# Kernel tuning notes

Measured on AMD Instinct MI355X. Metric: run time of the kernel, lower is better.

Reference implementation:

```python
import jax, jax.numpy as jnp
import numpy as np

DECAY = 0.9
BETA_OBS = 1.0
BETA_STATE = 1.0

N_OBS = 20000
N_STATES = 1024
N_ACTIONS = 64
STATE_DIM = 256
RFD = 2048


def setup_inputs() -> dict:
    key = jax.random.key(0)
    ks = jax.random.split(key, 7)
    Q = jax.random.normal(ks[0], (STATE_DIM, N_STATES), dtype=jnp.float32) / np.sqrt(STATE_DIM).astype(np.float32)
    V = jax.random.normal(ks[1], (STATE_DIM, N_ACTIONS), dtype=jnp.float32) / np.sqrt(STATE_DIM).astype(np.float32)
    W = jax.random.normal(ks[2], (RFD, STATE_DIM), dtype=jnp.float32)
    M_re = jax.random.normal(ks[3], (RFD, N_OBS), dtype=jnp.float32)
    M_im = jax.random.normal(ks[4], (RFD, N_OBS), dtype=jnp.float32)
    obs = jax.random.uniform(ks[5], (N_OBS,), dtype=jnp.float32)
    action = jax.random.uniform(ks[6], (N_ACTIONS,), dtype=jnp.float32)
    return {"Q": Q, "V": V, "W": W, "M_re": M_re, "M_im": M_im, "obs": obs, "action": action}


def reference(Q, V, W, M_re, M_im, obs, action):
    # One fused POCML step: memory write (decayed outer product), state
    # rotation via complex random-feature phase, clean_up (state-kernel
    # softmax retrieval), and obs retrieval from memory.
    D = W.shape[0]  # random_feature_dim
    M = M_re + 1j * M_im                       # [D, n_obs] complex64
    obs_c = obs.astype(jnp.complex64)
    # get_state_from_memory
    state0 = M @ obs_c                         # [D]
    # update_memory: M *= decay; M += outer(state, obs)
    M_new = DECAY * M + jnp.outer(state0, obs_c)
    # update_state: v = V @ action; phi_v = exp(1j * W @ v); state *= phi_v
    v = V @ action                             # [state_dim]
    phi_v = jnp.exp(1j * (W @ v))              # [D] complex64
    state1 = state0 * phi_v
    # clean_up: phi_Q = exp(1j * W @ Q), weights = softmax(beta*sim(phi_Q.T, state))
    phi_Q = jnp.exp(1j * (W @ Q))              # [D, n_states]
    score = BETA_STATE * (phi_Q.T @ jnp.conj(state1)).real / D  # [n_states]
    weights = jax.nn.softmax(score)
    state2 = phi_Q @ weights.astype(jnp.complex64)              # [D]
    # get_obs_from_memory: softmax(beta_obs * sim(M.T, state))
    obs_score = BETA_OBS * (M_new.T @ jnp.conj(state2)).real / D  # [n_obs]
    return jax.nn.softmax(obs_score)
```

## Files before the change

kernel.cpp:

```cpp
#include <hip/hip_runtime.h>
#include <math.h>

#define N_OBS    20000
#define N_OBS8   2500
#define N_STATES 1024
#define N_ACT    64
#define SDIM     256
#define RFD      2048
#define DECAY    0.9f
#define HALF_O8  1250
#define FLTMAX   3.402823466e+38f

typedef float v4f __attribute__((ext_vector_type(4)));
typedef float v2f __attribute__((ext_vector_type(2)));

__device__ __forceinline__ v4f ntload4(const float* p) {
    return __builtin_nontemporal_load((const v4f*)p);
}

__device__ __forceinline__ unsigned pk4_fp8(float a, float b, float c, float d) {
    unsigned w = __builtin_amdgcn_cvt_pk_fp8_f32(a, b, 0u, false);
    w = __builtin_amdgcn_cvt_pk_fp8_f32(c, d, w, true);
    return w;
}

#define OFF_SCORE  0
#define OFF_OBSACC 1024
#define OFF_DOT0   21024
#define ZERO_CNT   21028
#define OFF_P0RE   21028
#define OFF_P0IM   (OFF_P0RE + 2*RFD)
#define OFF_S2RE   (OFF_P0IM + 2*RFD)
#define OFF_S2IM   (OFF_S2RE + RFD)
#define OFF_VWS    (OFF_S2IM + RFD)
#define OFF_COSQ   (OFF_VWS + SDIM)
#define OFF_SINQ   (OFF_COSQ + RFD*N_STATES)
#define OFF_MH8    (OFF_SINQ + RFD*N_STATES)
#define MH8_FLOATS (RFD * N_OBS8 * 4)
#define WS_FLOATS  (OFF_MH8 + MH8_FLOATS)

#define NB_GEMM   512
#define NB_Z      21
#define NB_P1     (RFD * 2)
#define NB_FUSED  (NB_GEMM + 1 + NB_Z + NB_P1)

__global__ __launch_bounds__(256) void k_fused(
    const float* __restrict__ Mre, const float* __restrict__ Mim,
    const float* __restrict__ obs,
    const float* __restrict__ W, const float* __restrict__ Q,
    const float* __restrict__ V, const float* __restrict__ action,
    float* __restrict__ cosQ, float* __restrict__ sinQ,
    float* __restrict__ p0re, float* __restrict__ p0im,
    float* __restrict__ vout, uint4* __restrict__ Mh8,
    float* __restrict__ zbase)
{
    const int b = blockIdx.x;
    const int tid = threadIdx.x;

    if (b < NB_GEMM) {
        __shared__ float As[16][65];
        __shared__ float Bs[16][64];
        const int tx = tid & 15;
        const int ty = tid >> 4;
        const int m0 = (b >> 4) * 64;
        const int n0 = (b & 15) * 64;
        float c[4][4] = {};
        for (int k0 = 0; k0 < SDIM; k0 += 16) {
            {
                int k = tid & 15, mb = tid >> 4;
                #pragma unroll
                for (int j = 0; j < 4; j++)
                    As[k][mb + 16*j] = W[(size_t)(m0 + mb + 16*j) * SDIM + k0 + k];
            }
            {
                int n = tid & 63, kb = tid >> 6;
                #pragma unroll
                for (int j = 0; j < 4; j++)
                    Bs[kb + 4*j][n] = Q[(size_t)(k0 + kb + 4*j) * N_STATES + n0 + n];
            }
            __syncthreads();
            #pragma unroll
            for (int kk = 0; kk < 16; kk++) {
                float a[4], bb[4];
                #pragma unroll
                for (int i = 0; i < 4; i++) a[i] = As[kk][ty*4 + i];
                #pragma unroll
                for (int j = 0; j < 4; j++) bb[j] = Bs[kk][tx*4 + j];
                #pragma unroll
                for (int i = 0; i < 4; i++)
                    #pragma unroll
                    for (int j = 0; j < 4; j++)
                        c[i][j] += a[i] * bb[j];
            }
            __syncthreads();
        }
        #pragma unroll
        for (int i = 0; i < 4; i++) {
            int d = m0 + ty*4 + i;
            #pragma unroll
            for (int j = 0; j < 4; j++) {
                int s = n0 + tx*4 + j;
                float sn, cs;
                sincosf(c[i][j], &sn, &cs);
                cosQ[(size_t)d * N_STATES + s] = cs;
                sinQ[(size_t)d * N_STATES + s] = sn;
            }
        }
    } else if (b == NB_GEMM) {
        float acc = 0.f;
        for (int a = 0; a < N_ACT; a++) acc += V[tid * N_ACT + a] * action[a];
        vout[tid] = acc;
    } else if (b < NB_GEMM + 1 + NB_Z) {
        int idx = (b - (NB_GEMM + 1)) * 256 + tid;
        if (idx < ZERO_CNT / 4)
            ((float4*)zbase)[idx] = make_float4(0.f, 0.f, 0.f, 0.f);
    } else {
        const int p = b - (NB_GEMM + 1 + NB_Z);
        const int d = p >> 1;
        const int h = p & 1;
        const float* mr = Mre + (size_t)d * N_OBS;
        const float* mi = Mim + (size_t)d * N_OBS;
        uint4* mh = Mh8 + (size_t)d * N_OBS8;
        const float4* ob = (const float4*)obs;
        const int base = h * HALF_O8, lim = base + HALF_O8;
        float ar0 = 0.f, ar1 = 0.f, ai0 = 0.f, ai1 = 0.f;
        int i = base + tid;
        #pragma unroll
        for (int it = 0; it < 5; ++it, i += 256) {
            int ic = i < lim ? i : lim - 1;
            float4 oa = ob[2*ic], obv = ob[2*ic + 1];
            v4f ra = ntload4(mr + 8 * (size_t)ic);
            v4f rb = ntload4(mr + 8 * (size_t)ic + 4);
            v4f qa = ntload4(mi + 8 * (size_t)ic);
            v4f qb = ntload4(mi + 8 * (size_t)ic + 4);
            if (i < lim) {
                uint4 u;
                u.x = pk4_fp8(ra.x, qa.x, ra.y, qa.y);
                u.y = pk4_fp8(ra.z, qa.z, ra.w, qa.w);
                u.z = pk4_fp8(rb.x, qb.x, rb.y, qb.y);
                u.w = pk4_fp8(rb.z, qb.z, rb.w, qb.w);
                mh[ic] = u;
                ar0 += ra.x*oa.x + ra.y*oa.y + ra.z*oa.z + ra.w*oa.w;
                ar1 += rb.x*obv.x + rb.y*obv.y + rb.z*obv.z + rb.w*obv.w;
                ai0 += qa.x*oa.x + qa.y*oa.y + qa.z*oa.z + qa.w*oa.w;
                ai1 += qb.x*obv.x + qb.y*obv.y + qb.z*obv.z + qb.w*obv.w;
            }
        }
        float arr = ar0 + ar1;
        float aii = ai0 + ai1;
        #pragma unroll
        for (int off = 32; off > 0; off >>= 1) {
            arr += __shfl_down(arr, off);
            aii += __shfl_down(aii, off);
        }
        __shared__ float pr[4], pi[4];
        const int wave = tid >> 6, lane = tid & 63;
        if (lane == 0) { pr[wave] = arr; pi[wave] = aii; }
        __syncthreads();
        if (tid == 0) {
            p0re[h * RFD + d] = pr[0] + pr[1] + pr[2] + pr[3];
            p0im[h * RFD + d] = pi[0] + pi[1] + pi[2] + pi[3];
        }
    }
}

__global__ __launch_bounds__(256) void k_score(
    const float* __restrict__ cosQ, const float* __restrict__ sinQ,
    const float* __restrict__ W, const float* __restrict__ vws,
    const float* __restrict__ p0re, const float* __restrict__ p0im,
    float* __restrict__ score)
{
    __shared__ float s1r_s[32], s1i_s[32];
    const int tid = threadIdx.x;
    const int d0 = blockIdx.y * 32;
    {
        const int r = tid >> 3, g = tid & 7;
        const float4* wv4 = (const float4*)(W + (size_t)(d0 + r) * SDIM + g * 32);
        const float4* vv4 = (const float4*)(vws + g * 32);
        float th = 0.f;
        #pragma unroll
        for (int j = 0; j < 8; j++) {
            float4 wv = wv4[j], vv = vv4[j];
            th += wv.x*vv.x + wv.y*vv.y + wv.z*vv.z + wv.w*vv.w;
        }
        th += __shfl_xor(th, 4);
        th += __shfl_xor(th, 2);
        th += __shfl_xor(th, 1);
        if (g == 0) {
            const int d = d0 + r;
            float re = p0re[d] + p0re[RFD + d];
            float im = p0im[d] + p0im[RFD + d];
            float sn, cs;
            sincosf(th, &sn, &cs);
            s1r_s[r] = re * cs - im * sn;
            s1i_s[r] = re * sn + im * cs;
        }
    }
    __syncthreads();
    const int s = blockIdx.x * 256 + tid;
    float acc = 0.f;
    #pragma unroll 4
    for (int j = 0; j < 32; j++) {
        int d = d0 + j;
        acc += cosQ[(size_t)d * N_STATES + s] * s1r_s[j]
             + sinQ[(size_t)d * N_STATES + s] * s1i_s[j];
    }
    atomicAdd(&score[s], acc);
}

__global__ __launch_bounds__(256) void k_wst2(
    const float* __restrict__ cosQ, const float* __restrict__ sinQ,
    const float* __restrict__ score,
    const float* __restrict__ p0re, const float* __restrict__ p0im,
    float* __restrict__ s2re, float* __restrict__ s2im,
    float* __restrict__ dot0)
{
    __shared__ float red[256];
    __shared__ float r1[256], r2[256];
    const int b = blockIdx.x;
    const int tid = threadIdx.x;
    const float scale = 1.f / (float)RFD;
    float4 v = ((const float4*)score)[tid];
    v.x *= scale; v.y *= scale; v.z *= scale; v.w *= scale;
    float mx = fmaxf(fmaxf(v.x, v.y), fmaxf(v.z, v.w));
    red[tid] = mx; __syncthreads();
    for (int s = 128; s > 0; s >>= 1) {
        if (tid < s) red[tid] = fmaxf(red[tid], red[tid+s]);
        __syncthreads();
    }
    mx = red[0]; __syncthreads();
    float4 e;
    e.x = expf(v.x - mx); e.y = expf(v.y - mx);
    e.z = expf(v.z - mx); e.w = expf(v.w - mx);
    red[tid] = e.x + e.y + e.z + e.w; __syncthreads();
    for (int s = 128; s > 0; s >>= 1) {
        if (tid < s) red[tid] += red[tid+s];
        __syncthreads();
    }
    const float inv = 1.f / red[0];
    e.x *= inv; e.y *= inv; e.z *= inv; e.w *= inv;
    __syncthreads();
    float blockdot = 0.f;
    #pragma unroll
    for (int r = 0; r < 2; r++) {
        const int d = b * 2 + r;
        float4 a = ((const float4*)(cosQ + (size_t)d * N_STATES))[tid];
        float4 bb = ((const float4*)(sinQ + (size_t)d * N_STATES))[tid];
        r1[tid] = a.x*e.x + a.y*e.y + a.z*e.z + a.w*e.w;
        r2[tid] = bb.x*e.x + bb.y*e.y + bb.z*e.z + bb.w*e.w;
        __syncthreads();
        for (int s = 128; s > 0; s >>= 1) {
            if (tid < s) { r1[tid] += r1[tid+s]; r2[tid] += r2[tid+s]; }
            __syncthreads();
        }
        if (tid == 0) {
            s2re[d] = r1[0]; s2im[d] = r2[0];
            float s0r = p0re[d] + p0re[RFD + d];
            float s0i = p0im[d] + p0im[RFD + d];
            blockdot += s0r * r1[0] + s0i * r2[0];
        }
        __syncthreads();
    }
    if (tid == 0) atomicAdd(dot0, blockdot);
}

__global__ __launch_bounds__(256) void k_obs_acc8(
    const uint4* __restrict__ Mh8,
    const float* __restrict__ s2re, const float* __restrict__ s2im,
    float* __restrict__ obs_acc)
{
    __shared__ float c_s[32], s_s[32];
    const int tid = threadIdx.x;
    const int dbase = blockIdx.y * 32;
    if (tid < 32) { c_s[tid] = s2re[dbase + tid]; s_s[tid] = s2im[dbase + tid]; }
    __syncthreads();
    const int idx = blockIdx.x * 256 + tid;
    if (idx >= N_OBS8) return;
    const uint4* p = Mh8 + (size_t)dbase * N_OBS8 + idx;
    float a0 = 0.f, a1 = 0.f, a2 = 0.f, a3 = 0.f;
    float a4 = 0.f, a5 = 0.f, a6 = 0.f, a7 = 0.f;
    #pragma unroll 4
    for (int j = 0; j < 32; ++j) {
        uint4 u = p[(size_t)j * N_OBS8];
        float cc = c_s[j], ss = s_s[j];
        v2f f0 = __builtin_amdgcn_cvt_pk_f32_fp8(u.x, false);
        v2f f1 = __builtin_amdgcn_cvt_pk_f32_fp8(u.x, true);
        v2f f2 = __builtin_amdgcn_cvt_pk_f32_fp8(u.y, false);
        v2f f3 = __builtin_amdgcn_cvt_pk_f32_fp8(u.y, true);
        v2f f4 = __builtin_amdgcn_cvt_pk_f32_fp8(u.z, false);
        v2f f5 = __builtin_amdgcn_cvt_pk_f32_fp8(u.z, true);
        v2f f6 = __builtin_amdgcn_cvt_pk_f32_fp8(u.w, false);
        v2f f7 = __builtin_amdgcn_cvt_pk_f32_fp8(u.w, true);
        a0 += f0.x*cc + f0.y*ss;
        a1 += f1.x*cc + f1.y*ss;
        a2 += f2.x*cc + f2.y*ss;
        a3 += f3.x*cc + f3.y*ss;
        a4 += f4.x*cc + f4.y*ss;
        a5 += f5.x*cc + f5.y*ss;
        a6 += f6.x*cc + f6.y*ss;
        a7 += f7.x*cc + f7.y*ss;
    }
    float* dst = obs_acc + idx * 8;
    atomicAdd(dst + 0, a0);
    atomicAdd(dst + 1, a1);
    atomicAdd(dst + 2, a2);
    atomicAdd(dst + 3, a3);
    atomicAdd(dst + 4, a4);
    atomicAdd(dst + 5, a5);
    atomicAdd(dst + 6, a6);
    atomicAdd(dst + 7, a7);
}

__global__ __launch_bounds__(1024) void k_softmax_obs(
    const float* __restrict__ obs_acc, const float* __restrict__ obs,
    const float* __restrict__ dot0,
    float* __restrict__ out)
{
    __shared__ float red[1024];
    const int tid = threadIdx.x;
    const float d0 = dot0[0];
    const float scale = 1.f / (float)RFD;
    float vals[20];
    float mx = -FLTMAX;
    #pragma unroll
    for (int i = 0; i < 20; i++) {
        int idx = tid + i * 1024;
        if (idx < N_OBS) {
            float sc = (DECAY * obs_acc[idx] + obs[idx] * d0) * scale;
            vals[i] = sc;
            mx = fmaxf(mx, sc);
        } else vals[i] = -FLTMAX;
    }
    red[tid] = mx; __syncthreads();
    for (int s = 512; s > 0; s >>= 1) {
        if (tid < s) red[tid] = fmaxf(red[tid], red[tid+s]);
        __syncthreads();
    }
    mx = red[0]; __syncthreads();
    float sum = 0.f;
    #pragma unroll
    for (int i = 0; i < 20; i++) {
        int idx = tid + i * 1024;
        if (idx < N_OBS) {
            vals[i] = expf(vals[i] - mx);
            sum += vals[i];
        }
    }
    red[tid] = sum; __syncthreads();
    for (int s = 512; s > 0; s >>= 1) {
        if (tid < s) red[tid] += red[tid+s];
        __syncthreads();
    }
    const float inv = 1.f / red[0];
    #pragma unroll
    for (int i = 0; i < 20; i++) {
        int idx = tid + i * 1024;
        if (idx < N_OBS) out[idx] = vals[i] * inv;
    }
}

extern "C" void kernel_launch(void* const* d_in, const int* in_sizes, int n_in,
                              void* d_out, int out_size, void* d_ws, size_t ws_size,
                              hipStream_t stream) {
    const float* Q      = (const float*)d_in[0];
    const float* V      = (const float*)d_in[1];
    const float* W      = (const float*)d_in[2];
    const float* Mre    = (const float*)d_in[3];
    const float* Mim    = (const float*)d_in[4];
    const float* obs    = (const float*)d_in[5];
    const float* action = (const float*)d_in[6];
    float* out = (float*)d_out;
    float* ws  = (float*)d_ws;

    if (ws_size < (size_t)WS_FLOATS * sizeof(float)) return;

    float* score = ws + OFF_SCORE;
    float* oacc  = ws + OFF_OBSACC;
    float* dot0  = ws + OFF_DOT0;
    float* p0re  = ws + OFF_P0RE;
    float* p0im  = ws + OFF_P0IM;
    float* s2re  = ws + OFF_S2RE;
    float* s2im  = ws + OFF_S2IM;
    float* vws   = ws + OFF_VWS;
    float* cosQ  = ws + OFF_COSQ;
    float* sinQ  = ws + OFF_SINQ;
    uint4* Mh8   = (uint4*)(ws + OFF_MH8);

    k_fused<<<NB_FUSED, 256, 0, stream>>>(Mre, Mim, obs, W, Q, V, action,
                                          cosQ, sinQ, p0re, p0im, vws, Mh8, ws);
    k_score<<<dim3(4, 64), 256, 0, stream>>>(cosQ, sinQ, W, vws, p0re, p0im, score);
    k_wst2<<<RFD / 2, 256, 0, stream>>>(cosQ, sinQ, score, p0re, p0im,
                                        s2re, s2im, dot0);
    k_obs_acc8<<<dim3(10, 64), 256, 0, stream>>>(Mh8, s2re, s2im, oacc);
    k_softmax_obs<<<1, 1024, 0, stream>>>(oacc, obs, dot0, out);
}
```

Baseline: 440.4 us.

## Merge four tail kernels into one persistent kernel with grid barriers

Replaces the score, softmax/state2, obs-accumulate and final softmax kernels with a single 512-block kernel separated by software grid barriers built on atomic counter and generation words. The final softmax becomes a distributed two-pass reduction over 512 blocks instead of one 1024-thread block. This is meant to remove three launch gaps and the serial single-block softmax, at the cost of barrier spin overhead and a dependence on all 512 blocks being co-resident. The zeroing count is extended so the barrier counters and partial arrays are cleared by the earlier fused kernel.

```diff
diff --git a/kernel.cpp b/kernel.cpp
--- a/kernel.cpp
+++ b/kernel.cpp
@@ -27,8 +27,12 @@
 #define OFF_SCORE  0
 #define OFF_OBSACC 1024
 #define OFF_DOT0   21024
-#define ZERO_CNT   21028
-#define OFF_P0RE   21028
+#define OFF_CNT    21025
+#define OFF_GEN    21026
+#define OFF_PMAX   21028
+#define OFF_PSUM   (OFF_PMAX + 512)
+#define ZERO_CNT   (OFF_PSUM + 512)
+#define OFF_P0RE   22052
 #define OFF_P0IM   (OFF_P0RE + 2*RFD)
 #define OFF_S2RE   (OFF_P0IM + 2*RFD)
 #define OFF_S2IM   (OFF_S2RE + RFD)
@@ -40,7 +44,7 @@
 #define WS_FLOATS  (OFF_MH8 + MH8_FLOATS)
 
 #define NB_GEMM   512
-#define NB_Z      21
+#define NB_Z      22
 #define NB_P1     (RFD * 2)
 #define NB_FUSED  (NB_GEMM + 1 + NB_Z + NB_P1)
 
@@ -164,25 +168,66 @@
     }
 }
 
-__global__ __launch_bounds__(256) void k_score(
+#define NB_TAIL 512
+
+__device__ __forceinline__ void gridbar(unsigned* cnt, unsigned* gen) {
+    __syncthreads();
+    if (threadIdx.x == 0) {
+        __threadfence();
+        unsigned g = __hip_atomic_load(gen, __ATOMIC_RELAXED,
+                                       __HIP_MEMORY_SCOPE_AGENT);
+        unsigned a = __hip_atomic_fetch_add(cnt, 1u, __ATOMIC_ACQ_REL,
+                                            __HIP_MEMORY_SCOPE_AGENT);
+        if (a == NB_TAIL - 1) {
+            __hip_atomic_store(cnt, 0u, __ATOMIC_RELAXED,
+                               __HIP_MEMORY_SCOPE_AGENT);
+            __hip_atomic_fetch_add(gen, 1u, __ATOMIC_RELEASE,
+                                   __HIP_MEMORY_SCOPE_AGENT);
+        } else {
+            while (__hip_atomic_load(gen, __ATOMIC_ACQUIRE,
+                                     __HIP_MEMORY_SCOPE_AGENT) == g)
+                __builtin_amdgcn_s_sleep(1);
+        }
+        __threadfence();
+    }
+    __syncthreads();
+}
+
+__global__ __launch_bounds__(256, 4) void k_tail(
     const float* __restrict__ cosQ, const float* __restrict__ sinQ,
     const float* __restrict__ W, const float* __restrict__ vws,
     const float* __restrict__ p0re, const float* __restrict__ p0im,
-    float* __restrict__ score)
+    float* __restrict__ score,
+    float* __restrict__ s2re, float* __restrict__ s2im,
+    const uint4* __restrict__ Mh8,
+    const float* __restrict__ obs,
+    float* __restrict__ oacc, float* __restrict__ dot0,
+    unsigned* __restrict__ cnt, unsigned* __restrict__ gen,
+    float* __restrict__ pmax, float* __restrict__ psum,
+    float* __restrict__ out)
 {
-    __shared__ float s1r_s[32], s1i_s[32];
+    __shared__ float wts_s[1024];
+    __shared__ float red[256];
+    __shared__ float s1r_s[16], s1i_s[16];
+    __shared__ float cs_s[64], ss_s[64];
+    __shared__ float bd[4];
+    const int b = blockIdx.x;
     const int tid = threadIdx.x;
-    const int d0 = blockIdx.y * 32;
+    const float scale = 1.f / (float)RFD;
+
     {
-        const int r = tid >> 3, g = tid & 7;
-        const float4* wv4 = (const float4*)(W + (size_t)(d0 + r) * SDIM + g * 32);
-        const float4* vv4 = (const float4*)(vws + g * 32);
+        const int d0 = (b >> 2) * 16;
+        const int sc = b & 3;
+        const int r = tid >> 4, g = tid & 15;
+        const float4* wv4 = (const float4*)(W + (size_t)(d0 + r) * SDIM + g * 16);
+        const float4* vv4 = (const float4*)(vws + g * 16);
         float th = 0.f;
         #pragma unroll
-        for (int j = 0; j < 8; j++) {
+        for (int j = 0; j < 4; j++) {
             float4 wv = wv4[j], vv = vv4[j];
             th += wv.x*vv.x + wv.y*vv.y + wv.z*vv.z + wv.w*vv.w;
         }
+        th += __shfl_xor(th, 8);
         th += __shfl_xor(th, 4);
         th += __shfl_xor(th, 2);
         th += __shfl_xor(th, 1);
@@ -195,167 +240,161 @@
             s1r_s[r] = re * cs - im * sn;
             s1i_s[r] = re * sn + im * cs;
         }
-    }
-    __syncthreads();
-    const int s = blockIdx.x * 256 + tid;
-    float acc = 0.f;
-    #pragma unroll 4
-    for (int j = 0; j < 32; j++) {
-        int d = d0 + j;
-        acc += cosQ[(size_t)d * N_STATES + s] * s1r_s[j]
-             + sinQ[(size_t)d * N_STATES + s] * s1i_s[j];
-    }
-    atomicAdd(&score[s], acc);
-}
-
-__global__ __launch_bounds__(256) void k_wst2(
-    const float* __restrict__ cosQ, const float* __restrict__ sinQ,
-    const float* __restrict__ score,
-    const float* __restrict__ p0re, const float* __restrict__ p0im,
-    float* __restrict__ s2re, float* __restrict__ s2im,
-    float* __restrict__ dot0)
-{
-    __shared__ float red[256];
-    __shared__ float r1[256], r2[256];
-    const int b = blockIdx.x;
-    const int tid = threadIdx.x;
-    const float scale = 1.f / (float)RFD;
-    float4 v = ((const float4*)score)[tid];
-    v.x *= scale; v.y *= scale; v.z *= scale; v.w *= scale;
-    float mx = fmaxf(fmaxf(v.x, v.y), fmaxf(v.z, v.w));
-    red[tid] = mx; __syncthreads();
-    for (int s = 128; s > 0; s >>= 1) {
-        if (tid < s) red[tid] = fmaxf(red[tid], red[tid+s]);
-        __syncthreads();
-    }
-    mx = red[0]; __syncthreads();
-    float4 e;
-    e.x = expf(v.x - mx); e.y = expf(v.y - mx);
-    e.z = expf(v.z - mx); e.w = expf(v.w - mx);
-    red[tid] = e.x + e.y + e.z + e.w; __syncthreads();
-    for (int s = 128; s > 0; s >>= 1) {
-        if (tid < s) red[tid] += red[tid+s];
-        __syncthreads();
-    }
-    const float inv = 1.f / red[0];
-    e.x *= inv; e.y *= inv; e.z *= inv; e.w *= inv;
-    __syncthreads();
-    float blockdot = 0.f;
-    #pragma unroll
-    for (int r = 0; r < 2; r++) {
-        const int d = b * 2 + r;
-        float4 a = ((const float4*)(cosQ + (size_t)d * N_STATES))[tid];
-        float4 bb = ((const float4*)(sinQ + (size_t)d * N_STATES))[tid];
-        r1[tid] = a.x*e.x + a.y*e.y + a.z*e.z + a.w*e.w;
-        r2[tid] = bb.x*e.x + bb.y*e.y + bb.z*e.z + bb.w*e.w;
-        __syncthreads();
-        for (int s = 128; s > 0; s >>= 1) {
-            if (tid < s) { r1[tid] += r1[tid+s]; r2[tid] += r2[tid+s]; }
-            __syncthreads();
-        }
-        if (tid == 0) {
-            s2re[d] = r1[0]; s2im[d] = r2[0];
+        __syncthreads();
+        const int s = sc * 256 + tid;
+        float acc = 0.f;
+        #pragma unroll 4
+        for (int j = 0; j < 16; j++) {
+            int d = d0 + j;
+            acc += cosQ[(size_t)d * N_STATES + s] * s1r_s[j]
+                 + sinQ[(size_t)d * N_STATES + s] * s1i_s[j];
+        }
+        atomicAdd(&score[s], acc);
+    }
+    gridbar(cnt, gen);
+
+    {
+        float4 v = ((const float4*)score)[tid];
+        v.x *= scale; v.y *= scale; v.z *= scale; v.w *= scale;
+        float mx = fmaxf(fmaxf(v.x, v.y), fmaxf(v.z, v.w));
+        red[tid] = mx; __syncthreads();
+        for (int s = 128; s > 0; s >>= 1) {
+            if (tid < s) red[tid] = fmaxf(red[tid], red[tid+s]);
+            __syncthreads();
+        }
+        mx = red[0]; __syncthreads();
+        float4 e;
+        e.x = expf(v.x - mx); e.y = expf(v.y - mx);
+        e.z = expf(v.z - mx); e.w = expf(v.w - mx);
+        red[tid] = e.x + e.y + e.z + e.w; __syncthreads();
+        for (int s = 128; s > 0; s >>= 1) {
+            if (tid < s) red[tid] += red[tid+s];
+            __syncthreads();
+        }
+        const float inv = 1.f / red[0];
+        __syncthreads();
+        e.x *= inv; e.y *= inv; e.z *= inv; e.w *= inv;
+        ((float4*)wts_s)[tid] = e;
+        __syncthreads();
+        const int w = tid >> 6, l = tid & 63;
+        const int d = b * 4 + w;
+        float r1 = 0.f, r2 = 0.f;
+        const float* cr = cosQ + (size_t)d * N_STATES;
+        const float* sr = sinQ + (size_t)d * N_STATES;
+        #pragma unroll 4
+        for (int k = 0; k < 16; k++) {
+            float wt = wts_s[l + 64*k];
+            r1 += cr[l + 64*k] * wt;
+            r2 += sr[l + 64*k] * wt;
+        }
+        #pragma unroll
+        for (int off = 32; off > 0; off >>= 1) {
+            r1 += __shfl_xor(r1, off);
+            r2 += __shfl_xor(r2, off);
+        }
+        if (l == 0) {
+            s2re[d] = r1; s2im[d] = r2;
             float s0r = p0re[d] + p0re[RFD + d];
             float s0i = p0im[d] + p0im[RFD + d];
-            blockdot += s0r * r1[0] + s0i * r2[0];
-        }
-        __syncthreads();
-    }
-    if (tid == 0) atomicAdd(dot0, blockdot);
-}
-
-__global__ __launch_bounds__(256) void k_obs_acc8(
-    const uint4* __restrict__ Mh8,
-    const float* __restrict__ s2re, const float* __restrict__ s2im,
-    float* __restrict__ obs_acc)
-{
-    __shared__ float c_s[32], s_s[32];
-    const int tid = threadIdx.x;
-    const int dbase = blockIdx.y * 32;
-    if (tid < 32) { c_s[tid] = s2re[dbase + tid]; s_s[tid] = s2im[dbase + tid]; }
-    __syncthreads();
-    const int idx = blockIdx.x * 256 + tid;
-    if (idx >= N_OBS8) return;
-    const uint4* p = Mh8 + (size_t)dbase * N_OBS8 + idx;
-    float a0 = 0.f, a1 = 0.f, a2 = 0.f, a3 = 0.f;
-    float a4 = 0.f, a5 = 0.f, a6 = 0.f, a7 = 0.f;
-    #pragma unroll 4
-    for (int j = 0; j < 32; ++j) {
-        uint4 u = p[(size_t)j * N_OBS8];
-        float cc = c_s[j], ss = s_s[j];
-        v2f f0 = __builtin_amdgcn_cvt_pk_f32_fp8(u.x, false);
-        v2f f1 = __builtin_amdgcn_cvt_pk_f32_fp8(u.x, true);
-        v2f f2 = __builtin_amdgcn_cvt_pk_f32_fp8(u.y, false);
-        v2f f3 = __builtin_amdgcn_cvt_pk_f32_fp8(u.y, true);
-        v2f f4 = __builtin_amdgcn_cvt_pk_f32_fp8(u.z, false);
-        v2f f5 = __builtin_amdgcn_cvt_pk_f32_fp8(u.z, true);
-        v2f f6 = __builtin_amdgcn_cvt_pk_f32_fp8(u.w, false);
-        v2f f7 = __builtin_amdgcn_cvt_pk_f32_fp8(u.w, true);
-        a0 += f0.x*cc + f0.y*ss;
-        a1 += f1.x*cc + f1.y*ss;
-        a2 += f2.x*cc + f2.y*ss;
-        a3 += f3.x*cc + f3.y*ss;
-        a4 += f4.x*cc + f4.y*ss;
-        a5 += f5.x*cc + f5.y*ss;
-        a6 += f6.x*cc + f6.y*ss;
-        a7 += f7.x*cc + f7.y*ss;
-    }
-    float* dst = obs_acc + idx * 8;
-    atomicAdd(dst + 0, a0);
-    atomicAdd(dst + 1, a1);
-    atomicAdd(dst + 2, a2);
-    atomicAdd(dst + 3, a3);
-    atomicAdd(dst + 4, a4);
-    atomicAdd(dst + 5, a5);
-    atomicAdd(dst + 6, a6);
-    atomicAdd(dst + 7, a7);
-}
-
-__global__ __launch_bounds__(1024) void k_softmax_obs(
-    const float* __restrict__ obs_acc, const float* __restrict__ obs,
-    const float* __restrict__ dot0,
-    float* __restrict__ out)
-{
-    __shared__ float red[1024];
-    const int tid = threadIdx.x;
-    const float d0 = dot0[0];
-    const float scale = 1.f / (float)RFD;
-    float vals[20];
-    float mx = -FLTMAX;
-    #pragma unroll
-    for (int i = 0; i < 20; i++) {
-        int idx = tid + i * 1024;
-        if (idx < N_OBS) {
-            float sc = (DECAY * obs_acc[idx] + obs[idx] * d0) * scale;
-            vals[i] = sc;
-            mx = fmaxf(mx, sc);
-        } else vals[i] = -FLTMAX;
-    }
-    red[tid] = mx; __syncthreads();
-    for (int s = 512; s > 0; s >>= 1) {
-        if (tid < s) red[tid] = fmaxf(red[tid], red[tid+s]);
-        __syncthreads();
-    }
-    mx = red[0]; __syncthreads();
-    float sum = 0.f;
-    #pragma unroll
-    for (int i = 0; i < 20; i++) {
-        int idx = tid + i * 1024;
-        if (idx < N_OBS) {
-            vals[i] = expf(vals[i] - mx);
-            sum += vals[i];
-        }
-    }
-    red[tid] = sum; __syncthreads();
-    for (int s = 512; s > 0; s >>= 1) {
-        if (tid < s) red[tid] += red[tid+s];
-        __syncthreads();
-    }
-    const float inv = 1.f / red[0];
-    #pragma unroll
-    for (int i = 0; i < 20; i++) {
-        int idx = tid + i * 1024;
-        if (idx < N_OBS) out[idx] = vals[i] * inv;
+            bd[w] = s0r * r1 + s0i * r2;
+        }
+        __syncthreads();
+        if (tid == 0)
+            atomicAdd(dot0, (bd[0] + bd[1]) + (bd[2] + bd[3]));
+    }
+    gridbar(cnt, gen);
+
+    if (b < 320) {
+        const int colgrp = b % 10;
+        const int dbase = (b / 10) * 64;
+        if (tid < 64) { cs_s[tid] = s2re[dbase + tid]; ss_s[tid] = s2im[dbase + tid]; }
+        __syncthreads();
+        const int idx = colgrp * 256 + tid;
+        if (idx < N_OBS8) {
+            const uint4* p = Mh8 + (size_t)dbase * N_OBS8 + idx;
+            float a0 = 0.f, a1 = 0.f, a2 = 0.f, a3 = 0.f;
+            float a4 = 0.f, a5 = 0.f, a6 = 0.f, a7 = 0.f;
+            #pragma unroll 4
+            for (int j = 0; j < 64; ++j) {
+                uint4 u = p[(size_t)j * N_OBS8];
+                float cc = cs_s[j], ss = ss_s[j];
+                v2f f0 = __builtin_amdgcn_cvt_pk_f32_fp8(u.x, false);
+                v2f f1 = __builtin_amdgcn_cvt_pk_f32_fp8(u.x, true);
+                v2f f2 = __builtin_amdgcn_cvt_pk_f32_fp8(u.y, false);
+                v2f f3 = __builtin_amdgcn_cvt_pk_f32_fp8(u.y, true);
+                v2f f4 = __builtin_amdgcn_cvt_pk_f32_fp8(u.z, false);
+                v2f f5 = __builtin_amdgcn_cvt_pk_f32_fp8(u.z, true);
+                v2f f6 = __builtin_amdgcn_cvt_pk_f32_fp8(u.w, false);
+                v2f f7 = __builtin_amdgcn_cvt_pk_f32_fp8(u.w, true);
+                a0 += f0.x*cc + f0.y*ss;
+                a1 += f1.x*cc + f1.y*ss;
+                a2 += f2.x*cc + f2.y*ss;
+                a3 += f3.x*cc + f3.y*ss;
+                a4 += f4.x*cc + f4.y*ss;
+                a5 += f5.x*cc + f5.y*ss;
+                a6 += f6.x*cc + f6.y*ss;
+                a7 += f7.x*cc + f7.y*ss;
+            }
+            float* dst = oacc + idx * 8;
+            atomicAdd(dst + 0, a0);
+            atomicAdd(dst + 1, a1);
+            atomicAdd(dst + 2, a2);
+            atomicAdd(dst + 3, a3);
+            atomicAdd(dst + 4, a4);
+            atomicAdd(dst + 5, a5);
+            atomicAdd(dst + 6, a6);
+            atomicAdd(dst + 7, a7);
+        }
+    }
+    gridbar(cnt, gen);
+
+    const int o = b * 256 + tid;
+    const bool act = o < N_OBS;
+    {
+        float val = -FLTMAX;
+        if (act) {
+            val = (DECAY * oacc[o] + obs[o] * dot0[0]) * scale;
+            oacc[o] = val;
+        }
+        red[tid] = val; __syncthreads();
+        for (int s = 128; s > 0; s >>= 1) {
+            if (tid < s) red[tid] = fmaxf(red[tid], red[tid+s]);
+            __syncthreads();
+        }
+        if (tid == 0) pmax[b] = red[0];
+    }
+    gridbar(cnt, gen);
+
+    {
+        float m = fmaxf(pmax[tid], pmax[tid + 256]);
+        red[tid] = m; __syncthreads();
+        for (int s = 128; s > 0; s >>= 1) {
+            if (tid < s) red[tid] = fmaxf(red[tid], red[tid+s]);
+            __syncthreads();
+        }
+        const float gmax = red[0]; __syncthreads();
+        float e = 0.f;
+        if (act) {
+            e = expf(oacc[o] - gmax);
+            oacc[o] = e;
+        }
+        red[tid] = e; __syncthreads();
+        for (int s = 128; s > 0; s >>= 1) {
+            if (tid < s) red[tid] += red[tid+s];
+            __syncthreads();
+        }
+        if (tid == 0) psum[b] = red[0];
+    }
+    gridbar(cnt, gen);
+
+    {
+        red[tid] = psum[tid] + psum[tid + 256]; __syncthreads();
+        for (int s = 128; s > 0; s >>= 1) {
+            if (tid < s) red[tid] += red[tid+s];
+            __syncthreads();
+        }
+        const float inv = 1.f / red[0];
+        if (act) out[o] = oacc[o] * inv;
     }
 }
 
@@ -374,23 +413,25 @@
 
     if (ws_size < (size_t)WS_FLOATS * sizeof(float)) return;
 
-    float* score = ws + OFF_SCORE;
-    float* oacc  = ws + OFF_OBSACC;
-    float* dot0  = ws + OFF_DOT0;
-    float* p0re  = ws + OFF_P0RE;
-    float* p0im  = ws + OFF_P0IM;
-    float* s2re  = ws + OFF_S2RE;
-    float* s2im  = ws + OFF_S2IM;
-    float* vws   = ws + OFF_VWS;
-    float* cosQ  = ws + OFF_COSQ;
-    float* sinQ  = ws + OFF_SINQ;
-    uint4* Mh8   = (uint4*)(ws + OFF_MH8);
+    float*    score = ws + OFF_SCORE;
+    float*    oacc  = ws + OFF_OBSACC;
+    float*    dot0  = ws + OFF_DOT0;
+    unsigned* cnt   = (unsigned*)(ws + OFF_CNT);
+    unsigned* gen   = (unsigned*)(ws + OFF_GEN);
+    float*    pmax  = ws + OFF_PMAX;
+    float*    psum  = ws + OFF_PSUM;
+    float*    p0re  = ws + OFF_P0RE;
+    float*    p0im  = ws + OFF_P0IM;
+    float*    s2re  = ws + OFF_S2RE;
+    float*    s2im  = ws + OFF_S2IM;
+    float*    vws   = ws + OFF_VWS;
+    float*    cosQ  = ws + OFF_COSQ;
+    float*    sinQ  = ws + OFF_SINQ;
+    uint4*    Mh8   = (uint4*)(ws + OFF_MH8);
 
     k_fused<<<NB_FUSED, 256, 0, stream>>>(Mre, Mim, obs, W, Q, V, action,
                                           cosQ, sinQ, p0re, p0im, vws, Mh8, ws);
-    k_score<<<dim3(4, 64), 256, 0, stream>>>(cosQ, sinQ, W, vws, p0re, p0im, score);
-    k_wst2<<<RFD / 2, 256, 0, stream>>>(cosQ, sinQ, score, p0re, p0im,
-                                        s2re, s2im, dot0);
-    k_obs_acc8<<<dim3(10, 64), 256, 0, stream>>>(Mh8, s2re, s2im, oacc);
-    k_softmax_obs<<<1, 1024, 0, stream>>>(oacc, obs, dot0, out);
-}
+    k_tail<<<NB_TAIL, 256, 0, stream>>>(cosQ, sinQ, W, vws, p0re, p0im, score,
+                                        s2re, s2im, Mh8, obs, oacc, dot0,
+                                        cnt, gen, pmax, psum, out);
+}
```

New measurement: 808.8 us. 83.7% more time.
